# Performance work log

Measured on AMD Instinct MI355X. Metric: run time of the kernel, lower is better.

The kernel has to match this reference:

```python
import jax, jax.numpy as jnp
import numpy as np

_IDENTITY = jnp.array([1, 0, 0, 0], dtype=jnp.float32)

G, T, P, B = 512, 128, 256, 512  # num_graphs, max_terms, n_params, batch


def setup_inputs() -> dict:
    key = jax.random.key(0)
    k0, k1, k2, k3, k4 = jax.random.split(key, 5)
    psi_const = jax.random.randint(k0, (G, T), 0, 2).astype(jnp.int32)
    psi_params = jax.random.randint(k1, (G, T, P), 0, 2).astype(jnp.float32)
    phi_const = jax.random.randint(k2, (G, T), 0, 2).astype(jnp.int32)
    phi_params = jax.random.randint(k3, (G, T, P), 0, 2).astype(jnp.float32)
    param_vals = jax.random.randint(k4, (B, P), 0, 2).astype(jnp.float32)
    return {
        "psi_const": psi_const,
        "psi_params": psi_params,
        "phi_const": phi_const,
        "phi_params": phi_params,
        "param_vals": param_vals,
    }


def reference(psi_const, psi_params, phi_const, phi_params, param_vals):
    # GF(2) matmul: contract bitmasks with binary parameter values, mod 2.
    # psi_params: (G,T,P), param_vals: (B,P) -> (B,G,T)
    psi = jnp.mod(psi_const[None].astype(jnp.float32)
                  + jnp.einsum("gtp,bp->bgt", psi_params, param_vals), 2.0)
    phi = jnp.mod(phi_const[None].astype(jnp.float32)
                  + jnp.einsum("gtp,bp->bgt", phi_params, param_vals), 2.0)
    # Elementwise parity product and mod-2 sum over terms -> (B,G)
    exponent = jnp.mod(psi * phi, 2.0)
    sum_exponents = jnp.mod(jnp.sum(exponent, axis=-1), 2.0)
    # Parity-to-sign: (-1)^e = 1 - 2e, embedded as exact scalar (B,G,4)
    summands_exact = (1.0 - 2.0 * sum_exponents)[..., None] * _IDENTITY
    return summands_exact
```

## Files before the change

### kernel.cpp

```cpp
#include <hip/hip_runtime.h>

typedef unsigned long long u64;

#define G 512
#define T 128
#define P 256
#define B 512

#define PV_OFF    0
#define ROWS_OFF  16384
#define CODES_OFF (ROWS_OFF + (size_t)G * T * 8 * 8)
#define WS_NEEDED (CODES_OFF + (size_t)G * T * 4)


#define ROWS_TOTAL (G * T * 2)
#define TASKS      (ROWS_TOTAL + B)
#define TPW        16
#define PACK_BLOCKS (TASKS / (TPW * 4))

__global__ __launch_bounds__(256) void pack_all_kernel(
    const int*   __restrict__ psi_const,
    const float* __restrict__ psi_params,
    const int*   __restrict__ phi_const,
    const float* __restrict__ phi_params,
    const float* __restrict__ pv,
    u64*         __restrict__ rows_ws,
    unsigned*    __restrict__ codes_ws,
    u64*         __restrict__ pv_ws)
{
    int gtid = blockIdx.x * 256 + threadIdx.x;
    if (gtid < G * T) {
        unsigned pc = ((unsigned)psi_const[gtid]) & 1u;
        unsigned qc = ((unsigned)phi_const[gtid]) & 1u;
        codes_ws[gtid] = pc | (qc << 1);
    }

    const int lane = threadIdx.x & 63;
    const int wv   = (blockIdx.x << 2) | (threadIdx.x >> 6);
    const int base = wv * TPW;

    for (int i = 0; i < TPW; ++i) {
        int task = base + i;
        const float* src;
        u64* dst;
        if (task < ROWS_TOTAL) {
            int mat = task >> 16;
            int idx = task & (G * T - 1);
            src = (mat ? phi_params : psi_params) + (size_t)idx * P;
            dst = rows_ws + (size_t)idx * 8 + mat * 4;
        } else {
            int b = task - ROWS_TOTAL;
            src = pv + (size_t)b * P;
            dst = pv_ws + (size_t)b * 4;
        }
        float4 f = ((const float4*)src)[lane];
        u64 w0 = __ballot(f.x != 0.0f);
        u64 w1 = __ballot(f.y != 0.0f);
        u64 w2 = __ballot(f.z != 0.0f);
        u64 w3 = __ballot(f.w != 0.0f);
        if (lane == 0) {
            dst[0] = w0; dst[1] = w1; dst[2] = w2; dst[3] = w3;
        }
    }
}

__global__ __launch_bounds__(256) void pi_main2_kernel(
    const u64*      __restrict__ rows,
    const unsigned* __restrict__ codes,
    const u64*      __restrict__ pv,
    float4*         __restrict__ out)
{
    const int g = blockIdx.x >> 1;
    const int b = ((blockIdx.x & 1) << 8) | threadIdx.x;

    const u64* v = pv + (size_t)b * 4;
    u64 v0 = v[0], v1 = v[1], v2 = v[2], v3 = v[3];

    const u64*      Rg = rows  + (size_t)g * (T * 8);
    const unsigned* Cg = codes + g * T;

    unsigned e = 0;
    #pragma unroll 4
    for (int t = 0; t < T; ++t) {
        const u64* r = Rg + t * 8;
        u64 ma = (r[0] & v0) ^ (r[1] & v1) ^ (r[2] & v2) ^ (r[3] & v3);
        u64 mb = (r[4] & v0) ^ (r[5] & v1) ^ (r[6] & v2) ^ (r[7] & v3);
        unsigned c = Cg[t];
        e ^= (((unsigned)__popcll(ma) ^ c) & ((unsigned)__popcll(mb) ^ (c >> 1)));
    }
    e &= 1u;

    float s = 1.0f - 2.0f * (float)e;
    out[(size_t)b * G + g] = make_float4(s, 0.0f, 0.0f, 0.0f);
}

struct __align__(16) U64x2 { u64 x, y; };

__global__ __launch_bounds__(256) void pack_pv_kernel(
    const float* __restrict__ pv, u64* __restrict__ out)
{
    int lane = threadIdx.x & 63;
    int wave = threadIdx.x >> 6;
    int row  = blockIdx.x * 4 + wave;
    const float4* src = (const float4*)(pv + (size_t)row * P);
    float4 f = src[lane];
    u64 w0 = __ballot(f.x != 0.0f);
    u64 w1 = __ballot(f.y != 0.0f);
    u64 w2 = __ballot(f.z != 0.0f);
    u64 w3 = __ballot(f.w != 0.0f);
    if (lane == 0) {
        out[row * 4 + 0] = w0;
        out[row * 4 + 1] = w1;
        out[row * 4 + 2] = w2;
        out[row * 4 + 3] = w3;
    }
}

__global__ __launch_bounds__(512) void pi_main_kernel(
    const int*   __restrict__ psi_const,
    const float* __restrict__ psi_params,
    const int*   __restrict__ phi_const,
    const float* __restrict__ phi_params,
    const u64*   __restrict__ pv,
    float4*      __restrict__ out)
{
    __shared__ __align__(16) u64 rows[T * 8];
    __shared__ unsigned code_sm[T];

    const int g    = blockIdx.x;
    const int tid  = threadIdx.x;
    const int lane = tid & 63;
    const int wave = tid >> 6;

    if (tid < T) {
        unsigned pc = ((unsigned)psi_const[g * T + tid]) & 1u;
        unsigned qc = ((unsigned)phi_const[g * T + tid]) & 1u;
        code_sm[tid] = pc | (qc << 1);
    }

    for (int i = 0; i < 32; ++i) {
        int r = wave * 32 + i;
        int t = r & (T - 1);
        const float* mat = (r < T) ? psi_params : phi_params;
        int off = (r < T) ? 0 : 4;
        const float4* src = (const float4*)(mat + ((size_t)g * T + t) * P);
        float4 f = src[lane];
        u64 w0 = __ballot(f.x != 0.0f);
        u64 w1 = __ballot(f.y != 0.0f);
        u64 w2 = __ballot(f.z != 0.0f);
        u64 w3 = __ballot(f.w != 0.0f);
        if (lane == 0) {
            U64x2* d = (U64x2*)&rows[t * 8 + off];
            U64x2 a; a.x = w0; a.y = w1;
            U64x2 c; c.x = w2; c.y = w3;
            d[0] = a;
            d[1] = c;
        }
    }
    __syncthreads();

    const int b = tid;
    const u64* v = pv + (size_t)b * 4;
    u64 v0 = v[0], v1 = v[1], v2 = v[2], v3 = v[3];

    unsigned e = 0;
    #pragma unroll 8
    for (int t = 0; t < T; ++t) {
        const U64x2* row = (const U64x2*)&rows[t * 8];
        U64x2 p0 = row[0], p1 = row[1], q0 = row[2], q1 = row[3];
        u64 ma = (p0.x & v0) ^ (p0.y & v1) ^ (p1.x & v2) ^ (p1.y & v3);
        u64 mb = (q0.x & v0) ^ (q0.y & v1) ^ (q1.x & v2) ^ (q1.y & v3);
        unsigned c = code_sm[t];
        e ^= (((unsigned)__popcll(ma) ^ c) & ((unsigned)__popcll(mb) ^ (c >> 1)));
    }
    e &= 1u;

    float s = 1.0f - 2.0f * (float)e;
    out[(size_t)b * G + g] = make_float4(s, 0.0f, 0.0f, 0.0f);
}

extern "C" void kernel_launch(void* const* d_in, const int* in_sizes, int n_in,
                              void* d_out, int out_size, void* d_ws, size_t ws_size,
                              hipStream_t stream) {
    const int*   psi_const  = (const int*)  d_in[0];
    const float* psi_params = (const float*)d_in[1];
    const int*   phi_const  = (const int*)  d_in[2];
    const float* phi_params = (const float*)d_in[3];
    const float* param_vals = (const float*)d_in[4];

    if (ws_size >= WS_NEEDED) {
        u64*      pv_ws    = (u64*)((char*)d_ws + PV_OFF);
        u64*      rows_ws  = (u64*)((char*)d_ws + ROWS_OFF);
        unsigned* codes_ws = (unsigned*)((char*)d_ws + CODES_OFF);

        pack_all_kernel<<<PACK_BLOCKS, 256, 0, stream>>>(
            psi_const, psi_params, phi_const, phi_params, param_vals,
            rows_ws, codes_ws, pv_ws);
        pi_main2_kernel<<<G * 2, 256, 0, stream>>>(
            rows_ws, codes_ws, pv_ws, (float4*)d_out);
    } else {
        u64* pv_packed = (u64*)d_ws;
        pack_pv_kernel<<<B / 4, 256, 0, stream>>>(param_vals, pv_packed);
        pi_main_kernel<<<G, 512, 0, stream>>>(psi_const, psi_params,
                                              phi_const, phi_params,
                                              pv_packed, (float4*)d_out);
    }
}
```

Before: 194.1 us.

## Transpose main GF(2) kernel to hold term rows in registers and batch uniform loads

```diff
diff --git a/kernel.cpp b/kernel.cpp
--- a/kernel.cpp
+++ b/kernel.cpp
@@ -14,9 +14,10 @@
 
 
 #define ROWS_TOTAL (G * T * 2)
-#define TASKS      (ROWS_TOTAL + B)
-#define TPW        16
-#define PACK_BLOCKS (TASKS / (TPW * 4))
+#define TPW        8
+#define ROW_BLOCKS (ROWS_TOTAL / (TPW * 4))
+#define PV_BLOCKS  (B / (TPW * 4))
+#define PACK_BLOCKS (ROW_BLOCKS + PV_BLOCKS)
 
 __global__ __launch_bounds__(256) void pack_all_kernel(
     const int*   __restrict__ psi_const,
@@ -36,62 +37,111 @@
     }
 
     const int lane = threadIdx.x & 63;
-    const int wv   = (blockIdx.x << 2) | (threadIdx.x >> 6);
-    const int base = wv * TPW;
-
+    const int wvin = threadIdx.x >> 6;
+
+    const float* srcb;
+    u64*         dstb;
+    size_t       dst_stride;
+    if (blockIdx.x < ROW_BLOCKS) {
+        int base = (blockIdx.x * 4 + wvin) * TPW;
+        int mat  = base >> 16;
+        int idx  = base & (G * T - 1);
+        srcb = (mat ? phi_params : psi_params) + (size_t)idx * P;
+        dstb = rows_ws + (size_t)idx * 8 + mat * 4;
+        dst_stride = 8;
+    } else {
+        int brow = ((blockIdx.x - ROW_BLOCKS) * 4 + wvin) * TPW;
+        srcb = pv + (size_t)brow * P;
+        dstb = pv_ws + (size_t)brow * 4;
+        dst_stride = 4;
+    }
+
+    const float4* src = (const float4*)srcb;
+    float4 f[TPW];
+    #pragma unroll
+    for (int i = 0; i < TPW; ++i)
+        f[i] = src[i * (P / 4) + lane];
+
+    u64 w[TPW][4];
+    #pragma unroll
     for (int i = 0; i < TPW; ++i) {
-        int task = base + i;
-        const float* src;
-        u64* dst;
-        if (task < ROWS_TOTAL) {
-            int mat = task >> 16;
-            int idx = task & (G * T - 1);
-            src = (mat ? phi_params : psi_params) + (size_t)idx * P;
-            dst = rows_ws + (size_t)idx * 8 + mat * 4;
-        } else {
-            int b = task - ROWS_TOTAL;
-            src = pv + (size_t)b * P;
-            dst = pv_ws + (size_t)b * 4;
-        }
-        float4 f = ((const float4*)src)[lane];
-        u64 w0 = __ballot(f.x != 0.0f);
-        u64 w1 = __ballot(f.y != 0.0f);
-        u64 w2 = __ballot(f.z != 0.0f);
-        u64 w3 = __ballot(f.w != 0.0f);
-        if (lane == 0) {
-            dst[0] = w0; dst[1] = w1; dst[2] = w2; dst[3] = w3;
-        }
-    }
-}
-
-__global__ __launch_bounds__(256) void pi_main2_kernel(
+        w[i][0] = __ballot(f[i].x != 0.0f);
+        w[i][1] = __ballot(f[i].y != 0.0f);
+        w[i][2] = __ballot(f[i].z != 0.0f);
+        w[i][3] = __ballot(f[i].w != 0.0f);
+    }
+
+    if (lane == 0) {
+        #pragma unroll
+        for (int i = 0; i < TPW; ++i) {
+            ulonglong2* d = (ulonglong2*)(dstb + (size_t)i * dst_stride);
+            d[0] = make_ulonglong2(w[i][0], w[i][1]);
+            d[1] = make_ulonglong2(w[i][2], w[i][3]);
+        }
+    }
+}
+
+__global__ __launch_bounds__(512) void pi_trans_kernel(
     const u64*      __restrict__ rows,
     const unsigned* __restrict__ codes,
     const u64*      __restrict__ pv,
     float4*         __restrict__ out)
 {
-    const int g = blockIdx.x >> 1;
-    const int b = ((blockIdx.x & 1) << 8) | threadIdx.x;
-
-    const u64* v = pv + (size_t)b * 4;
-    u64 v0 = v[0], v1 = v[1], v2 = v[2], v3 = v[3];
-
-    const u64*      Rg = rows  + (size_t)g * (T * 8);
-    const unsigned* Cg = codes + g * T;
-
-    unsigned e = 0;
-    #pragma unroll 4
-    for (int t = 0; t < T; ++t) {
-        const u64* r = Rg + t * 8;
-        u64 ma = (r[0] & v0) ^ (r[1] & v1) ^ (r[2] & v2) ^ (r[3] & v3);
-        u64 mb = (r[4] & v0) ^ (r[5] & v1) ^ (r[6] & v2) ^ (r[7] & v3);
-        unsigned c = Cg[t];
-        e ^= (((unsigned)__popcll(ma) ^ c) & ((unsigned)__popcll(mb) ^ (c >> 1)));
-    }
-    e &= 1u;
-
-    float s = 1.0f - 2.0f * (float)e;
-    out[(size_t)b * G + g] = make_float4(s, 0.0f, 0.0f, 0.0f);
+    const int g    = blockIdx.x;
+    const int lane = threadIdx.x & 63;
+    const int wv   = threadIdx.x >> 6;
+
+    const u64* Rg = rows + (size_t)g * (T * 8);
+
+    u64 ra[8], rb[8];
+    {
+        const ulonglong2* p0 = (const ulonglong2*)(Rg + (size_t)lane * 8);
+        const ulonglong2* p1 = (const ulonglong2*)(Rg + (size_t)(lane + 64) * 8);
+        #pragma unroll
+        for (int q = 0; q < 4; ++q) { ulonglong2 x = p0[q]; ra[2*q] = x.x; ra[2*q+1] = x.y; }
+        #pragma unroll
+        for (int q = 0; q < 4; ++q) { ulonglong2 x = p1[q]; rb[2*q] = x.x; rb[2*q+1] = x.y; }
+    }
+    unsigned ca = codes[g * T + lane];
+    unsigned cb = codes[g * T + lane + 64];
+    unsigned pa = ca & 1u, qa = (ca >> 1) & 1u;
+    unsigned pb = cb & 1u, qb = (cb >> 1) & 1u;
+
+    #pragma unroll
+    for (int grp = 0; grp < 2; ++grp) {
+        int b0  = wv * 64 + grp * 32;
+        int b0u = __builtin_amdgcn_readfirstlane(b0);
+        const u64* vp = pv + (size_t)b0u * 4;
+
+        unsigned acc = 0;
+        #pragma unroll
+        for (int i = 0; i < 32; ++i) {
+            u64 v0 = vp[i * 4 + 0], v1 = vp[i * 4 + 1];
+            u64 v2 = vp[i * 4 + 2], v3 = vp[i * 4 + 3];
+            u64 m0 = (ra[0] & v0) ^ (ra[1] & v1) ^ (ra[2] & v2) ^ (ra[3] & v3);
+            u64 m1 = (ra[4] & v0) ^ (ra[5] & v1) ^ (ra[6] & v2) ^ (ra[7] & v3);
+            u64 m2 = (rb[0] & v0) ^ (rb[1] & v1) ^ (rb[2] & v2) ^ (rb[3] & v3);
+            u64 m3 = (rb[4] & v0) ^ (rb[5] & v1) ^ (rb[6] & v2) ^ (rb[7] & v3);
+            unsigned f0 = (unsigned)m0 ^ (unsigned)(m0 >> 32);
+            unsigned f1 = (unsigned)m1 ^ (unsigned)(m1 >> 32);
+            unsigned f2 = (unsigned)m2 ^ (unsigned)(m2 >> 32);
+            unsigned f3 = (unsigned)m3 ^ (unsigned)(m3 >> 32);
+            unsigned t01 = ((unsigned)__popc(f0) ^ pa) & ((unsigned)__popc(f1) ^ qa);
+            unsigned t23 = ((unsigned)__popc(f2) ^ pb) & ((unsigned)__popc(f3) ^ qb);
+            acc ^= ((t01 ^ t23) & 1u) << i;
+        }
+
+        unsigned red = acc;
+        #pragma unroll
+        for (int m = 1; m < 64; m <<= 1)
+            red ^= __shfl_xor(red, m, 64);
+
+        if (lane < 32) {
+            int b = b0u + lane;
+            float s = 1.0f - 2.0f * (float)((red >> lane) & 1u);
+            out[(size_t)b * G + g] = make_float4(s, 0.0f, 0.0f, 0.0f);
+        }
+    }
 }
 
 struct __align__(16) U64x2 { u64 x, y; };
@@ -196,7 +246,7 @@
         pack_all_kernel<<<PACK_BLOCKS, 256, 0, stream>>>(
             psi_const, psi_params, phi_const, phi_params, param_vals,
             rows_ws, codes_ws, pv_ws);
-        pi_main2_kernel<<<G * 2, 256, 0, stream>>>(
+        pi_trans_kernel<<<G, 512, 0, stream>>>(
             rows_ws, codes_ws, pv_ws, (float4*)d_out);
     } else {
         u64* pv_packed = (u64*)d_ws;
```

Measured after the change: 188.3 us. 1.03x faster.
